# Kernel tuning notes

Hardware: AMD Instinct MI355X
Metric: run time of the kernel (lower is better)

## Reference

```python
import jax, jax.numpy as jnp
import numpy as np

HID = 1024
NH = 4  # heads for GAT conv1 and all attention blocks
FF = 2048
SLOPE = 0.2


def _ln(x, g, b):
    m = x.mean(-1, keepdims=True)
    v = ((x - m) ** 2).mean(-1, keepdims=True)
    return (x - m) / jnp.sqrt(v + 1e-5) * g + b


def _mha(q, k, v, in_w, in_b, out_w, out_b, nh):
    # q:[B,Lq,E], k/v:[B,Lk,E]; torch MultiheadAttention math (eval mode)
    B, Lq, E = q.shape
    hd = E // nh
    wq, wk, wv = jnp.split(in_w, 3, axis=0)
    bq, bk, bv = jnp.split(in_b, 3)
    qh = (q @ wq.T + bq).reshape(B, Lq, nh, hd)
    kh = (k @ wk.T + bk).reshape(B, -1, nh, hd)
    vh = (v @ wv.T + bv).reshape(B, -1, nh, hd)
    s = jnp.einsum('bqhd,bkhd->bhqk', qh, kh) / jnp.sqrt(jnp.asarray(hd, q.dtype))
    a = jax.nn.softmax(s, axis=-1)
    o = jnp.einsum('bhqk,bkhd->bqhd', a, vh).reshape(B, Lq, E)
    return o @ out_w.T + out_b


def _gatv2(x, edge_index, w_l, b_l, w_r, b_r, att, bias, heads, out_ch):
    # PyG GATv2Conv, flow='target_to_source': i (aggregation dst) = edge_index[0], j = edge_index[1]
    n = x.shape[0]
    dst = edge_index[0]
    src = edge_index[1]
    x_l = (x @ w_l + b_l).reshape(n, heads, out_ch)
    x_r = (x @ w_r + b_r).reshape(n, heads, out_ch)
    msg = x_l[src]                                   # [E,H,C] gathered source features
    e = jax.nn.leaky_relu(msg + x_r[dst], SLOPE)     # [E,H,C]
    alpha = (e * att).sum(-1)                        # [E,H]
    amax = jax.ops.segment_max(alpha, dst, num_segments=n)
    alpha = jnp.exp(alpha - amax[dst])
    denom = jax.ops.segment_sum(alpha, dst, num_segments=n)
    alpha = alpha / (denom[dst] + 1e-16)
    out = jax.ops.segment_sum(msg * alpha[..., None], dst, num_segments=n)
    return out.reshape(n, heads * out_ch) + bias


def setup_inputs() -> dict:
    key = jax.random.key(0)
    ks = iter(jax.random.split(key, 64))
    N, DF, B, L, E_rand = 8000, 768, 32, 14, 96000
    w = lambda *s: jax.random.normal(next(ks), s, jnp.float32) * 0.02
    z = lambda *s: jnp.zeros(s, jnp.float32)
    o = lambda *s: jnp.ones(s, jnp.float32)
    ei = jax.random.randint(next(ks), (2, E_rand), 0, N, jnp.int32)
    self_loops = jnp.tile(jnp.arange(N, dtype=jnp.int32)[None, :], (2, 1))
    inp = {
        'img_feat': jax.random.normal(next(ks), (B, HID), jnp.float32),
        'node_features': jax.random.normal(next(ks), (N, DF), jnp.float32),
        'edge_index': jnp.concatenate([ei, self_loops], axis=1),
        'target_idx': jax.random.randint(next(ks), (L,), 0, N, jnp.int32),
        # GATv2 conv1: 768 -> 4 heads x 256
        'gat1_wl': w(DF, HID), 'gat1_bl': z(HID), 'gat1_wr': w(DF, HID), 'gat1_br': z(HID),
        'gat1_att': w(NH, HID // NH), 'gat1_bias': z(HID),
        # GATv2 conv2: 1024 -> 1 head x 1024
        'gat2_wl': w(HID, HID), 'gat2_bl': z(HID), 'gat2_wr': w(HID, HID), 'gat2_br': z(HID),
        'gat2_att': w(1, HID), 'gat2_bias': z(HID),
        # cross-modal MHA + FFN layer
        'xa_in_w': w(3 * HID, HID), 'xa_in_b': z(3 * HID), 'xa_out_w': w(HID, HID), 'xa_out_b': z(HID),
        'xl_l1_w': w(FF, HID), 'xl_l1_b': z(FF), 'xl_l2_w': w(HID, FF), 'xl_l2_b': z(HID),
        'xl_n1_g': o(HID), 'xl_n1_b': z(HID), 'xl_n2_g': o(HID), 'xl_n2_b': z(HID),
        # 2-layer TransformerEncoder (stacked leading dim = layer)
        'enc_in_w': w(2, 3 * HID, HID), 'enc_in_b': z(2, 3 * HID),
        'enc_out_w': w(2, HID, HID), 'enc_out_b': z(2, HID),
        'enc_l1_w': w(2, FF, HID), 'enc_l1_b': z(2, FF),
        'enc_l2_w': w(2, HID, FF), 'enc_l2_b': z(2, HID),
        'enc_n1_g': o(2, HID), 'enc_n1_b': z(2, HID),
        'enc_n2_g': o(2, HID), 'enc_n2_b': z(2, HID),
        'cls_w': w(1, HID), 'cls_b': z(1),
    }
    return inp


def reference(img_feat, node_features, edge_index, target_idx,
              gat1_wl, gat1_bl, gat1_wr, gat1_br, gat1_att, gat1_bias,
              gat2_wl, gat2_bl, gat2_wr, gat2_br, gat2_att, gat2_bias,
              xa_in_w, xa_in_b, xa_out_w, xa_out_b,
              xl_l1_w, xl_l1_b, xl_l2_w, xl_l2_b, xl_n1_g, xl_n1_b, xl_n2_g, xl_n2_b,
              enc_in_w, enc_in_b, enc_out_w, enc_out_b, enc_l1_w, enc_l1_b, enc_l2_w, enc_l2_b,
              enc_n1_g, enc_n1_b, enc_n2_g, enc_n2_b, cls_w, cls_b):
    x = _gatv2(node_features, edge_index, gat1_wl, gat1_bl, gat1_wr, gat1_br, gat1_att, gat1_bias, NH, HID // NH)
    x = jax.nn.leaky_relu(x, SLOPE)
    x = _gatv2(x, edge_index, gat2_wl, gat2_bl, gat2_wr, gat2_br, gat2_att, gat2_bias, 1, HID)
    t = x[target_idx]                                  # [L, HID]
    B = img_feat.shape[0]
    L = t.shape[0]
    q = jnp.broadcast_to(t[None], (B, L, HID))
    kv = img_feat[:, None, :]                          # [B, 1, HID]
    attn = _mha(q, kv, kv, xa_in_w, xa_in_b, xa_out_w, xa_out_b, NH)
    src = _ln(t[None] + attn, xl_n1_g, xl_n1_b)
    ff = jax.nn.relu(src @ xl_l1_w.T + xl_l1_b) @ xl_l2_w.T + xl_l2_b
    src = _ln(src + ff, xl_n2_g, xl_n2_b)
    for i in range(2):  # TransformerEncoder, post-norm, relu, eval mode
        a = _mha(src, src, src, enc_in_w[i], enc_in_b[i], enc_out_w[i], enc_out_b[i], NH)
        src = _ln(src + a, enc_n1_g[i], enc_n1_b[i])
        f = jax.nn.relu(src @ enc_l1_w[i].T + enc_l1_b[i]) @ enc_l2_w[i].T + enc_l2_b[i]
        src = _ln(src + f, enc_n2_g[i], enc_n2_b[i])
    return (src @ cls_w.T + cls_b)[..., 0]             # [B, L]
```

## Files before the change

kernel.cpp:

```cpp
#include <hip/hip_runtime.h>
#include <hip/hip_bf16.h>

typedef __bf16 bf16;
typedef bf16 bf16x8 __attribute__((ext_vector_type(8)));
typedef bf16 bf16x4 __attribute__((ext_vector_type(4)));
typedef float f32x4 __attribute__((ext_vector_type(4)));

#define HID 1024
#define FFD 2048

typedef __attribute__((address_space(3))) void lds_void;
typedef const __attribute__((address_space(1))) void gm_void;

__device__ __forceinline__ void gload_lds16(const bf16* g, bf16* l)
{
    __builtin_amdgcn_global_load_lds((gm_void*)g, (lds_void*)l, 16, 0, 0);
}

__global__ __launch_bounds__(256) void cvt_bf16_kernel(
    const float* __restrict__ src, bf16* __restrict__ dst, long n)
{
    long i = ((long)blockIdx.x * 256 + threadIdx.x) * 4;
    if (i >= n) return;
    float4 f = *(const float4*)&src[i];
    bf16x4 v = {(bf16)f.x, (bf16)f.y, (bf16)f.z, (bf16)f.w};
    *(bf16x4*)&dst[i] = v;
}

__global__ __launch_bounds__(256) void cvt_t_bf16_kernel(
    const float* __restrict__ in, bf16* __restrict__ out, int R, int C)
{
    __shared__ bf16 tile[32][33];
    const int c0 = blockIdx.x * 32, r0 = blockIdx.y * 32;
    const int tx = threadIdx.x & 31, ty = threadIdx.x >> 5;
#pragma unroll
    for (int i = ty; i < 32; i += 8)
        tile[i][tx] = (bf16)in[(long)(r0 + i) * C + c0 + tx];
    __syncthreads();
#pragma unroll
    for (int i = ty; i < 32; i += 8)
        out[(long)(c0 + i) * R + r0 + tx] = tile[tx][i];
}

template <int ACT, int OUTBF16>
__global__ __launch_bounds__(256) void gemm_bf16_kernel(
    const bf16* __restrict__ A, const bf16* __restrict__ B,
    const float* __restrict__ bias, void* __restrict__ Cp,
    int M, int N, int K, int NB)
{
    const int total = gridDim.x;
    const int h = blockIdx.x;
    const int t = (total % 8 == 0) ? ((h & 7) * (total >> 3) + (h >> 3)) : h;
    const int bn = t % NB, bm = t / NB;

    const int tid  = threadIdx.x;
    const int lane = tid & 63, wave = tid >> 6;
    const int wr   = wave >> 1, wc = wave & 1;

    __shared__ bf16 As[128][32];
    __shared__ bf16 Bs[128][32];

    f32x4 acc[4][4] = {};

    const int srow = wave * 16 + (lane >> 2);
    const int scol = (lane & 3) << 3;
    const long ga0 = (long)min(bm * 128 + srow,      M - 1) * K + scol;
    const long ga1 = (long)min(bm * 128 + srow + 64, M - 1) * K + scol;
    const long gb0 = (long)(bn * 128 + srow)      * K + scol;
    const long gb1 = (long)(bn * 128 + srow + 64) * K + scol;
    bf16* ldsA0 = &As[0][0] + wave * 512;
    bf16* ldsA1 = &As[0][0] + 2048 + wave * 512;
    bf16* ldsB0 = &Bs[0][0] + wave * 512;
    bf16* ldsB1 = &Bs[0][0] + 2048 + wave * 512;

    const int quad = lane >> 4;
    const int mr   = lane & 15;
    const int kf   = quad * 8;

    for (int k0 = 0; k0 < K; k0 += 32) {
        gload_lds16(A + ga0 + k0, ldsA0);
        gload_lds16(A + ga1 + k0, ldsA1);
        gload_lds16(B + gb0 + k0, ldsB0);
        gload_lds16(B + gb1 + k0, ldsB1);
        __syncthreads();

        bf16x8 af[4], bfr[4];
#pragma unroll
        for (int i = 0; i < 4; ++i) af[i]  = *(const bf16x8*)&As[wr * 64 + i * 16 + mr][kf];
#pragma unroll
        for (int j = 0; j < 4; ++j) bfr[j] = *(const bf16x8*)&Bs[wc * 64 + j * 16 + mr][kf];
#pragma unroll
        for (int i = 0; i < 4; ++i)
#pragma unroll
            for (int j = 0; j < 4; ++j)
                acc[i][j] = __builtin_amdgcn_mfma_f32_16x16x32_bf16(af[i], bfr[j], acc[i][j], 0, 0, 0);
        __syncthreads();
    }

    const int crow = quad * 4;
#pragma unroll
    for (int i = 0; i < 4; ++i) {
#pragma unroll
        for (int j = 0; j < 4; ++j) {
            const int   col = bn * 128 + wc * 64 + j * 16 + mr;
            const float bv  = bias[col];
#pragma unroll
            for (int r = 0; r < 4; ++r) {
                const int row = bm * 128 + wr * 64 + i * 16 + crow + r;
                if (row < M) {
                    float v = acc[i][j][r] + bv;
                    if (ACT == 1) v = fmaxf(v, 0.f);
                    if (OUTBF16) ((bf16*)Cp)[(long)row * N + col] = (bf16)v;
                    else         ((float*)Cp)[(long)row * N + col] = v;
                }
            }
        }
    }
}

template <int KS>
__global__ __launch_bounds__(256) void gemm_sk_kernel(
    const float* __restrict__ A, const float* __restrict__ Bt,
    float* __restrict__ part, int M, int N, int K)
{
    const int tid  = threadIdx.x;
    const int bn   = blockIdx.x, bm = blockIdx.y, kz = blockIdx.z;
    const int lane = tid & 63, wave = tid >> 6;
    const int wr   = wave >> 1, wc = wave & 1;

    __shared__ bf16 As[128][40];
    __shared__ bf16 Bs[128][40];

    f32x4 acc[4][4] = {};

    const int  lr = tid >> 2;
    const int  lc = (tid & 3) << 3;
    const long a0 = (long)min(bm * 128 + lr,      M - 1) * K;
    const long a1 = (long)min(bm * 128 + lr + 64, M - 1) * K;
    const long b0 = (long)(bn * 128 + lr)      * K;
    const long b1 = (long)(bn * 128 + lr + 64) * K;

    const int quad = lane >> 4;
    const int mr   = lane & 15;
    const int kf   = quad * 8;

    const int Kc   = K / KS;
    const int kbeg = kz * Kc, kend = kbeg + Kc;

    float4 ra[4], rb[4];
    auto load_chunk = [&](int k0) {
        ra[0] = *(const float4*)&A[a0 + k0 + lc];
        ra[1] = *(const float4*)&A[a0 + k0 + lc + 4];
        ra[2] = *(const float4*)&A[a1 + k0 + lc];
        ra[3] = *(const float4*)&A[a1 + k0 + lc + 4];
        rb[0] = *(const float4*)&Bt[b0 + k0 + lc];
        rb[1] = *(const float4*)&Bt[b0 + k0 + lc + 4];
        rb[2] = *(const float4*)&Bt[b1 + k0 + lc];
        rb[3] = *(const float4*)&Bt[b1 + k0 + lc + 4];
    };

    load_chunk(kbeg);
    for (int k0 = kbeg; k0 < kend; k0 += 32) {
        {
            bf16x8 v0 = {(bf16)ra[0].x,(bf16)ra[0].y,(bf16)ra[0].z,(bf16)ra[0].w,
                         (bf16)ra[1].x,(bf16)ra[1].y,(bf16)ra[1].z,(bf16)ra[1].w};
            *(bf16x8*)&As[lr][lc] = v0;
            bf16x8 v1 = {(bf16)ra[2].x,(bf16)ra[2].y,(bf16)ra[2].z,(bf16)ra[2].w,
                         (bf16)ra[3].x,(bf16)ra[3].y,(bf16)ra[3].z,(bf16)ra[3].w};
            *(bf16x8*)&As[lr + 64][lc] = v1;
            bf16x8 v2 = {(bf16)rb[0].x,(bf16)rb[0].y,(bf16)rb[0].z,(bf16)rb[0].w,
                         (bf16)rb[1].x,(bf16)rb[1].y,(bf16)rb[1].z,(bf16)rb[1].w};
            *(bf16x8*)&Bs[lr][lc] = v2;
            bf16x8 v3 = {(bf16)rb[2].x,(bf16)rb[2].y,(bf16)rb[2].z,(bf16)rb[2].w,
                         (bf16)rb[3].x,(bf16)rb[3].y,(bf16)rb[3].z,(bf16)rb[3].w};
            *(bf16x8*)&Bs[lr + 64][lc] = v3;
        }
        __syncthreads();
        if (k0 + 32 < kend) load_chunk(k0 + 32);

        bf16x8 af[4], bfr[4];
#pragma unroll
        for (int i = 0; i < 4; ++i) af[i]  = *(const bf16x8*)&As[wr * 64 + i * 16 + mr][kf];
#pragma unroll
        for (int j = 0; j < 4; ++j) bfr[j] = *(const bf16x8*)&Bs[wc * 64 + j * 16 + mr][kf];
#pragma unroll
        for (int i = 0; i < 4; ++i)
#pragma unroll
            for (int j = 0; j < 4; ++j)
                acc[i][j] = __builtin_amdgcn_mfma_f32_16x16x32_bf16(af[i], bfr[j], acc[i][j], 0, 0, 0);
        __syncthreads();
    }

    const int crow = quad * 4;
    float* dst = part + (size_t)kz * M * N;
#pragma unroll
    for (int i = 0; i < 4; ++i) {
#pragma unroll
        for (int j = 0; j < 4; ++j) {
            const int col = bn * 128 + wc * 64 + j * 16 + mr;
#pragma unroll
            for (int r = 0; r < 4; ++r) {
                const int row = bm * 128 + wr * 64 + i * 16 + crow + r;
                if (row < M) dst[(long)row * N + col] = acc[i][j][r];
            }
        }
    }
}

template <int ACT, int KS>
__global__ __launch_bounds__(256) void sk_reduce_kernel(
    const float* __restrict__ part, const float* __restrict__ bias,
    float* __restrict__ C, long MN, int N)
{
    long i = ((long)blockIdx.x * 256 + threadIdx.x) * 4;
    if (i >= MN) return;
    float4 s = *(const float4*)&part[i];
#pragma unroll
    for (int k = 1; k < KS; ++k) {
        float4 p = *(const float4*)&part[(size_t)k * MN + i];
        s.x += p.x; s.y += p.y; s.z += p.z; s.w += p.w;
    }
    const int col = (int)(i % N);
    float4 bv = *(const float4*)&bias[col];
    s.x += bv.x; s.y += bv.y; s.z += bv.z; s.w += bv.w;
    if (ACT) {
        s.x = fmaxf(s.x, 0.f); s.y = fmaxf(s.y, 0.f);
        s.z = fmaxf(s.z, 0.f); s.w = fmaxf(s.w, 0.f);
    }
    *(float4*)&C[i] = s;
}

__device__ __forceinline__ void ln_finish(float v[4], int c0, const float* g,
                                          const float* beta, float* outrow)
{
    float s1 = v[0] + v[1] + v[2] + v[3];
    float s2 = v[0] * v[0] + v[1] * v[1] + v[2] * v[2] + v[3] * v[3];
    __shared__ float red[8];
    for (int o = 32; o; o >>= 1) { s1 += __shfl_down(s1, o); s2 += __shfl_down(s2, o); }
    const int wave = threadIdx.x >> 6, lane = threadIdx.x & 63;
    if (lane == 0) { red[wave] = s1; red[4 + wave] = s2; }
    __syncthreads();
    if (threadIdx.x == 0) {
        red[0] += red[1] + red[2] + red[3];
        red[4] += red[5] + red[6] + red[7];
    }
    __syncthreads();
    const float mean = red[0] * (1.f / HID);
    const float var  = fmaxf(red[4] * (1.f / HID) - mean * mean, 0.f);
    const float rstd = rsqrtf(var + 1e-5f);
#pragma unroll
    for (int k = 0; k < 4; ++k) {
        int c = c0 + k;
        outrow[c] = (v[k] - mean) * rstd * g[c] + beta[c];
    }
}

template <int KS>
__global__ __launch_bounds__(256) void sk_reduce_ln_kernel(
    const float* __restrict__ part, const float* __restrict__ bias,
    float* __restrict__ srcio, const float* __restrict__ g,
    const float* __restrict__ beta, long MN)
{
    const long row = blockIdx.x;
    const int c0 = threadIdx.x * 4;
    const long base = row * HID + c0;
    float4 s = *(const float4*)&part[base];
#pragma unroll
    for (int k = 1; k < KS; ++k) {
        float4 p = *(const float4*)&part[(size_t)k * MN + base];
        s.x += p.x; s.y += p.y; s.z += p.z; s.w += p.w;
    }
    float4 bv = *(const float4*)&bias[c0];
    float4 rv = *(const float4*)&srcio[base];
    float v[4] = {s.x + bv.x + rv.x, s.y + bv.y + rv.y,
                  s.z + bv.z + rv.z, s.w + bv.w + rv.w};
    ln_finish(v, c0, g, beta, srcio + row * HID);
}

__global__ void zero_i32_kernel(int* __restrict__ p, int n)
{
    int i = blockIdx.x * 256 + threadIdx.x;
    if (i < n) p[i] = 0;
}

__global__ void hist_kernel(const int* __restrict__ ei, int E, int* __restrict__ deg)
{
    int e = blockIdx.x * 256 + threadIdx.x;
    if (e < E) atomicAdd(&deg[ei[e]], 1);
}

__global__ void scan_kernel(const int* __restrict__ deg, int* __restrict__ rowstart,
                            int* __restrict__ cursor, int n)
{
    __shared__ int sm[1024];
    __shared__ int carry;
    if (threadIdx.x == 0) carry = 0;
    __syncthreads();
    for (int base = 0; base < n; base += 1024) {
        int i = base + threadIdx.x;
        int v = (i < n) ? deg[i] : 0;
        sm[threadIdx.x] = v;
        __syncthreads();
        for (int off = 1; off < 1024; off <<= 1) {
            int t = (threadIdx.x >= off) ? sm[threadIdx.x - off] : 0;
            __syncthreads();
            sm[threadIdx.x] += t;
            __syncthreads();
        }
        if (i < n) { int ex = carry + sm[threadIdx.x] - v; rowstart[i] = ex; cursor[i] = ex; }
        __syncthreads();
        if (threadIdx.x == 0) carry += sm[1023];
        __syncthreads();
    }
    if (threadIdx.x == 0) rowstart[n] = carry;
}

__global__ void scatter_kernel(const int* __restrict__ ei, int E,
                               int* __restrict__ cursor, int* __restrict__ eidx)
{
    int e = blockIdx.x * 256 + threadIdx.x;
    if (e < E) { int p = atomicAdd(&cursor[ei[e]], 1); eidx[p] = e; }
}

template <int NH, int LRELU, int OUTBF16>
__global__ __launch_bounds__(256) void gat_wave_kernel(
    const bf16* __restrict__ xl, const bf16* __restrict__ xr,
    const float* __restrict__ att,
    const int* __restrict__ ei, const int* __restrict__ rowstart,
    const int* __restrict__ eidx, const float* __restrict__ bias,
    void* __restrict__ outp, int E, int Nn)
{
    const int wave = threadIdx.x >> 6, lane = threadIdx.x & 63;
    const int n = blockIdx.x * 4 + wave;
    if (n >= Nn) return;

    const int rs = rowstart[n];
    int deg = rowstart[n + 1] - rs;
    if (deg > 128) deg = 128;

    int my_src = ei[E + eidx[min(rs + lane, E - 1)]];
    int my_src2 = 0;
    if (deg > 64) my_src2 = ei[E + eidx[min(rs + 64 + lane, E - 1)]];

    const int c0 = lane * 16;
    float xrf[16], av[16];
    {
        bf16x8 r0 = *(const bf16x8*)&xr[(long)n * HID + c0];
        bf16x8 r1 = *(const bf16x8*)&xr[(long)n * HID + c0 + 8];
#pragma unroll
        for (int t = 0; t < 8; ++t) { xrf[t] = (float)r0[t]; xrf[8 + t] = (float)r1[t]; }
        float4 t0 = *(const float4*)&att[c0],     t1 = *(const float4*)&att[c0 + 4];
        float4 t2 = *(const float4*)&att[c0 + 8], t3 = *(const float4*)&att[c0 + 12];
        av[0]=t0.x; av[1]=t0.y; av[2]=t0.z;  av[3]=t0.w;
        av[4]=t1.x; av[5]=t1.y; av[6]=t1.z;  av[7]=t1.w;
        av[8]=t2.x; av[9]=t2.y; av[10]=t2.z; av[11]=t2.w;
        av[12]=t3.x; av[13]=t3.y; av[14]=t3.z; av[15]=t3.w;
    }

    float m = -1e30f, s = 0.f;
    float acc[16];
#pragma unroll
    for (int t = 0; t < 16; ++t) acc[t] = 0.f;

    int sj = __shfl(my_src, 0);
    bf16x8 na0 = *(const bf16x8*)&xl[(long)sj * HID + c0];
    bf16x8 na1 = *(const bf16x8*)&xl[(long)sj * HID + c0 + 8];

    for (int j = 0; j < deg; ++j) {
        bf16x8 x0 = na0, x1 = na1;
        if (j + 1 < deg) {
            int msrc = (j + 1 < 64) ? my_src : my_src2;
            int sn = __shfl(msrc, (j + 1) & 63);
            na0 = *(const bf16x8*)&xl[(long)sn * HID + c0];
            na1 = *(const bf16x8*)&xl[(long)sn * HID + c0 + 8];
        }
        float xf[16];
#pragma unroll
        for (int t = 0; t < 8; ++t) { xf[t] = (float)x0[t]; xf[8 + t] = (float)x1[t]; }
        float partial = 0.f;
#pragma unroll
        for (int t = 0; t < 16; ++t) {
            float v = xf[t] + xrf[t];
            v = v > 0.f ? v : 0.2f * v;
            partial += v * av[t];
        }
        const int RW = (NH == 4) ? 16 : 64;
#pragma unroll
        for (int o = 1; o < RW; o <<= 1) partial += __shfl_xor(partial, o);
        float mn = fmaxf(m, partial);
        float f = __expf(m - mn);
        float p = __expf(partial - mn);
        s = s * f + p;
#pragma unroll
        for (int t = 0; t < 16; ++t) acc[t] = acc[t] * f + p * xf[t];
        m = mn;
    }

    const float dinv = 1.f / (s + 1e-16f);
    float bv[16];
    {
        float4 t0 = *(const float4*)&bias[c0],     t1 = *(const float4*)&bias[c0 + 4];
        float4 t2 = *(const float4*)&bias[c0 + 8], t3 = *(const float4*)&bias[c0 + 12];
        bv[0]=t0.x; bv[1]=t0.y; bv[2]=t0.z;  bv[3]=t0.w;
        bv[4]=t1.x; bv[5]=t1.y; bv[6]=t1.z;  bv[7]=t1.w;
        bv[8]=t2.x; bv[9]=t2.y; bv[10]=t2.z; bv[11]=t2.w;
        bv[12]=t3.x; bv[13]=t3.y; bv[14]=t3.z; bv[15]=t3.w;
    }
    float ov[16];
#pragma unroll
    for (int t = 0; t < 16; ++t) {
        float v = acc[t] * dinv + bv[t];
        if (LRELU) v = v > 0.f ? v : 0.2f * v;
        ov[t] = v;
    }
    if (OUTBF16) {
        bf16x8 w0, w1;
#pragma unroll
        for (int t = 0; t < 8; ++t) { w0[t] = (bf16)ov[t]; w1[t] = (bf16)ov[8 + t]; }
        *(bf16x8*)&((bf16*)outp)[(long)n * HID + c0] = w0;
        *(bf16x8*)&((bf16*)outp)[(long)n * HID + c0 + 8] = w1;
    } else {
        float* op = (float*)outp + (long)n * HID + c0;
#pragma unroll
        for (int t = 0; t < 4; ++t) {
            float4 w = {ov[t * 4], ov[t * 4 + 1], ov[t * 4 + 2], ov[t * 4 + 3]};
            *(float4*)&op[t * 4] = w;
        }
    }
}

__global__ __launch_bounds__(256) void ln_cross_kernel(
    const float* __restrict__ x2, const int* __restrict__ tidx,
    const float* __restrict__ attnb, const float* __restrict__ g,
    const float* __restrict__ beta, float* __restrict__ out, int L)
{
    const int row = blockIdx.x;
    const int b = row / L, l = row - b * L;
    const long tr = (long)tidx[l] * HID, ar = (long)b * HID;
    const int c0 = threadIdx.x * 4;
    float v[4];
#pragma unroll
    for (int k = 0; k < 4; ++k)
        v[k] = x2[tr + c0 + k] + attnb[ar + c0 + k];
    ln_finish(v, c0, g, beta, out + (long)row * HID);
}

__global__ __launch_bounds__(256) void self_attn_kernel(
    const float* __restrict__ qkv, float* __restrict__ out, int L)
{
    const int b = blockIdx.x >> 2, h = blockIdx.x & 3;
    const int tid = threadIdx.x;
    __shared__ float q[16][256], kk[16][256], vv[16][256];
    __shared__ float sc[16][16];
    for (int i = tid; i < L * 256; i += 256) {
        const int l = i >> 8, d = i & 255;
        const long rb = (long)(b * L + l) * 3072 + h * 256 + d;
        q[l][d]  = qkv[rb];
        kk[l][d] = qkv[rb + 1024];
        vv[l][d] = qkv[rb + 2048];
    }
    __syncthreads();
    if (tid < L * L) {
        const int l1 = tid / L, l2 = tid - l1 * L;
        float s = 0.f;
        for (int d = 0; d < 256; ++d) s += q[l1][d] * kk[l2][d];
        sc[l1][l2] = s * 0.0625f;
    }
    __syncthreads();
    if (tid < L) {
        float mx = -1e30f;
        for (int j = 0; j < L; ++j) mx = fmaxf(mx, sc[tid][j]);
        float ssum = 0.f;
        for (int j = 0; j < L; ++j) { float e = expf(sc[tid][j] - mx); sc[tid][j] = e; ssum += e; }
        const float inv = 1.f / ssum;
        for (int j = 0; j < L; ++j) sc[tid][j] *= inv;
    }
    __syncthreads();
    for (int l1 = 0; l1 < L; ++l1) {
        float a = 0.f;
        for (int l2 = 0; l2 < L; ++l2) a += sc[l1][l2] * vv[l2][tid];
        out[(long)(b * L + l1) * HID + h * 256 + tid] = a;
    }
}

__global__ __launch_bounds__(256) void cls_kernel(
    const float* __restrict__ src, const float* __restrict__ w,
    const float* __restrict__ b, float* __restrict__ out, int rows)
{
    const int row = blockIdx.x * 4 + (threadIdx.x >> 6);
    const int lane = threadIdx.x & 63;
    if (row >= rows) return;
    float s = 0.f;
    for (int c = lane; c < HID; c += 64) s += src[(long)row * HID + c] * w[c];
    for (int o = 32; o; o >>= 1) s += __shfl_down(s, o);
    if (lane == 0) out[row] = s + b[0];
}

extern "C" void kernel_launch(void* const* d_in, const int* in_sizes, int n_in,
                              void* d_out, int out_size, void* d_ws, size_t ws_size,
                              hipStream_t stream)
{
    const float* img_feat      = (const float*)d_in[0];
    const float* node_features = (const float*)d_in[1];
    const int*   edge_index    = (const int*)d_in[2];
    const int*   target_idx    = (const int*)d_in[3];
    const float* gat1_wl  = (const float*)d_in[4];
    const float* gat1_bl  = (const float*)d_in[5];
    const float* gat1_wr  = (const float*)d_in[6];
    const float* gat1_br  = (const float*)d_in[7];
    const float* gat1_att = (const float*)d_in[8];
    const float* gat1_bias= (const float*)d_in[9];
    const float* gat2_wl  = (const float*)d_in[10];
    const float* gat2_bl  = (const float*)d_in[11];
    const float* gat2_wr  = (const float*)d_in[12];
    const float* gat2_br  = (const float*)d_in[13];
    const float* gat2_att = (const float*)d_in[14];
    const float* gat2_bias= (const float*)d_in[15];
    const float* xa_in_w  = (const float*)d_in[16];
    const float* xa_in_b  = (const float*)d_in[17];
    const float* xa_out_w = (const float*)d_in[18];
    const float* xa_out_b = (const float*)d_in[19];
    const float* xl_l1_w  = (const float*)d_in[20];
    const float* xl_l1_b  = (const float*)d_in[21];
    const float* xl_l2_w  = (const float*)d_in[22];
    const float* xl_l2_b  = (const float*)d_in[23];
    const float* xl_n1_g  = (const float*)d_in[24];
    const float* xl_n1_b  = (const float*)d_in[25];
    const float* xl_n2_g  = (const float*)d_in[26];
    const float* xl_n2_b  = (const float*)d_in[27];
    const float* enc_in_w = (const float*)d_in[28];
    const float* enc_in_b = (const float*)d_in[29];
    const float* enc_out_w= (const float*)d_in[30];
    const float* enc_out_b= (const float*)d_in[31];
    const float* enc_l1_w = (const float*)d_in[32];
    const float* enc_l1_b = (const float*)d_in[33];
    const float* enc_l2_w = (const float*)d_in[34];
    const float* enc_l2_b = (const float*)d_in[35];
    const float* enc_n1_g = (const float*)d_in[36];
    const float* enc_n1_b = (const float*)d_in[37];
    const float* enc_n2_g = (const float*)d_in[38];
    const float* enc_n2_b = (const float*)d_in[39];
    const float* cls_w    = (const float*)d_in[40];
    const float* cls_b    = (const float*)d_in[41];

    const int DF = in_sizes[4] / HID;
    const int Nn = in_sizes[1] / DF;
    const int E  = in_sizes[2] / 2;
    const int L  = in_sizes[3];
    const int B  = in_sizes[0] / HID;
    const int R  = B * L;

    char* basep = (char*)d_ws;
    size_t off = 0;
    auto alloc = [&](size_t bytes) -> char* {
        char* r = basep + off; off += (bytes + 255) & ~(size_t)255; return r;
    };
    size_t regA_need = 0;
    {
        auto sz = [&](size_t b) { regA_need += (b + 255) & ~(size_t)255; };
        sz((size_t)Nn * DF * 2); sz((size_t)DF * HID * 2); sz((size_t)DF * HID * 2);
        sz((size_t)HID * HID * 2); sz((size_t)HID * HID * 2); sz((size_t)Nn * HID * 2);
    }
    size_t regA_bytes = regA_need > (size_t)Nn * HID * 4 ? regA_need : (size_t)Nn * HID * 4;
    char* regionA = alloc(regA_bytes);
    {
        size_t aoff = 0;
        auto allocA = [&](size_t bytes) -> char* {
            char* r = regionA + aoff; aoff += (bytes + 255) & ~(size_t)255; return r;
        };
        bf16* nfb  = (bf16*)allocA((size_t)Nn * DF * 2);
        bf16* w1lT = (bf16*)allocA((size_t)DF * HID * 2);
        bf16* w1rT = (bf16*)allocA((size_t)DF * HID * 2);
        bf16* w2lT = (bf16*)allocA((size_t)HID * HID * 2);
        bf16* w2rT = (bf16*)allocA((size_t)HID * HID * 2);
        bf16* x1   = (bf16*)allocA((size_t)Nn * HID * 2);

        float* x2  = (float*)regionA;

        bf16* xlb = (bf16*)alloc((size_t)Nn * HID * 2);
        bf16* xrb = (bf16*)alloc((size_t)Nn * HID * 2);
        int*   deg      = (int*)alloc((size_t)Nn * 4);
        int*   rowstart = (int*)alloc((size_t)(Nn + 1) * 4);
        int*   cursor   = (int*)alloc((size_t)(Nn + 1) * 4);
        int*   eidx     = (int*)alloc((size_t)E * 4);
        float* skpart   = (float*)alloc((size_t)8 * R * 3 * HID * 4);

        char* qb = (char*)xlb; size_t qoff = 0;
        auto alloc2 = [&](size_t bytes) -> char* {
            char* r = qb + qoff; qoff += (bytes + 255) & ~(size_t)255; return r;
        };
        float* vproj  = (float*)alloc2((size_t)B * HID * 4);
        float* attnb  = (float*)alloc2((size_t)B * HID * 4);
        float* srcbuf = (float*)alloc2((size_t)R * HID * 4);
        float* h1buf  = (float*)alloc2((size_t)R * FFD * 4);
        float* ffbuf  = (float*)alloc2((size_t)R * HID * 4);
        float* qkvbuf = (float*)alloc2((size_t)R * 3 * HID * 4);

        const int gE  = (E + 255) / 256;
        const int gMn = (Nn + 127) / 128;
        const long MNr = (long)R * HID;

        auto gemm_sk4 = [&](const float* A, const float* Bt, const float* bias,
                            float* C, int M, int N, int K, int act) {
            gemm_sk_kernel<4><<<dim3(N / 128, (M + 127) / 128, 4), 256, 0, stream>>>(
                A, Bt, skpart, M, N, K);
            long MN = (long)M * N;
            int g = (int)((MN / 4 + 255) / 256);
            if (act) sk_reduce_kernel<1,4><<<g, 256, 0, stream>>>(skpart, bias, C, MN, N);
            else     sk_reduce_kernel<0,4><<<g, 256, 0, stream>>>(skpart, bias, C, MN, N);
        };
        auto gemm_sk8 = [&](const float* A, const float* Bt, const float* bias,
                            float* C, int M, int N, int K, int act) {
            gemm_sk_kernel<8><<<dim3(N / 128, (M + 127) / 128, 8), 256, 0, stream>>>(
                A, Bt, skpart, M, N, K);
            long MN = (long)M * N;
            int g = (int)((MN / 4 + 255) / 256);
            if (act) sk_reduce_kernel<1,8><<<g, 256, 0, stream>>>(skpart, bias, C, MN, N);
            else     sk_reduce_kernel<0,8><<<g, 256, 0, stream>>>(skpart, bias, C, MN, N);
        };
        auto gemm_sk8_ln = [&](const float* A, const float* Bt, const float* bias,
                               float* srcio, const float* g, const float* beta, int K) {
            gemm_sk_kernel<8><<<dim3(HID / 128, (R + 127) / 128, 8), 256, 0, stream>>>(
                A, Bt, skpart, R, HID, K);
            sk_reduce_ln_kernel<8><<<R, 256, 0, stream>>>(skpart, bias, srcio, g, beta, MNr);
        };

        zero_i32_kernel<<<(Nn + 255) / 256, 256, 0, stream>>>(deg, Nn);
        hist_kernel<<<gE, 256, 0, stream>>>(edge_index, E, deg);
        scan_kernel<<<1, 1024, 0, stream>>>(deg, rowstart, cursor, Nn);
        scatter_kernel<<<gE, 256, 0, stream>>>(edge_index, E, cursor, eidx);

        cvt_bf16_kernel<<<(int)(((long)Nn * DF / 4 + 255) / 256), 256, 0, stream>>>(
            node_features, nfb, (long)Nn * DF);
        cvt_t_bf16_kernel<<<dim3(HID / 32, DF / 32), 256, 0, stream>>>(gat1_wl, w1lT, DF, HID);
        cvt_t_bf16_kernel<<<dim3(HID / 32, DF / 32), 256, 0, stream>>>(gat1_wr, w1rT, DF, HID);
        cvt_t_bf16_kernel<<<dim3(HID / 32, HID / 32), 256, 0, stream>>>(gat2_wl, w2lT, HID, HID);
        cvt_t_bf16_kernel<<<dim3(HID / 32, HID / 32), 256, 0, stream>>>(gat2_wr, w2rT, HID, HID);

        gemm_bf16_kernel<0,1><<<8 * gMn, 256, 0, stream>>>(nfb, w1lT, gat1_bl, xlb, Nn, HID, DF, 8);
        gemm_bf16_kernel<0,1><<<8 * gMn, 256, 0, stream>>>(nfb, w1rT, gat1_br, xrb, Nn, HID, DF, 8);
        gat_wave_kernel<4,1,1><<<(Nn + 3) / 4, 256, 0, stream>>>(
            xlb, xrb, gat1_att, edge_index, rowstart, eidx, gat1_bias, x1, E, Nn);

        gemm_bf16_kernel<0,1><<<8 * gMn, 256, 0, stream>>>(x1, w2lT, gat2_bl, xlb, Nn, HID, HID, 8);
        gemm_bf16_kernel<0,1><<<8 * gMn, 256, 0, stream>>>(x1, w2rT, gat2_br, xrb, Nn, HID, HID, 8);
        gat_wave_kernel<1,0,0><<<(Nn + 3) / 4, 256, 0, stream>>>(
            xlb, xrb, gat2_att, edge_index, rowstart, eidx, gat2_bias, x2, E, Nn);

        gemm_sk8(img_feat, xa_in_w + (size_t)2 * HID * HID, xa_in_b + 2 * HID, vproj, B, HID, HID, 0);
        gemm_sk8(vproj, xa_out_w, xa_out_b, attnb, B, HID, HID, 0);
        ln_cross_kernel<<<R, 256, 0, stream>>>(x2, target_idx, attnb, xl_n1_g, xl_n1_b, srcbuf, L);

        gemm_sk4(srcbuf, xl_l1_w, xl_l1_b, h1buf, R, FFD, HID, 1);
        gemm_sk8_ln(h1buf, xl_l2_w, xl_l2_b, srcbuf, xl_n2_g, xl_n2_b, FFD);

        for (int i = 0; i < 2; ++i) {
            gemm_sk4(srcbuf, enc_in_w + (size_t)i * 3 * HID * HID, enc_in_b + i * 3 * HID,
                     qkvbuf, R, 3 * HID, HID, 0);
            self_attn_kernel<<<B * 4, 256, 0, stream>>>(qkvbuf, ffbuf, L);
            gemm_sk8_ln(ffbuf, enc_out_w + (size_t)i * HID * HID, enc_out_b + i * HID,
                        srcbuf, enc_n1_g + i * HID, enc_n1_b + i * HID, HID);
            gemm_sk4(srcbuf, enc_l1_w + (size_t)i * FFD * HID, enc_l1_b + i * FFD,
                     h1buf, R, FFD, HID, 1);
            gemm_sk8_ln(h1buf, enc_l2_w + (size_t)i * HID * FFD, enc_l2_b + i * HID,
                        srcbuf, enc_n2_g + i * HID, enc_n2_b + i * HID, FFD);
        }

        cls_kernel<<<(R + 3) / 4, 256, 0, stream>>>(srcbuf, cls_w, cls_b, (float*)d_out, R);
    }
}
```

Before: 696.6 us.

## Restrict GATv2 layers to the two-hop neighborhood of target nodes

Only the target rows of the second GAT layer feed the rest of the model. The change builds one-hop and two-hop frontiers from the CSR adjacency, compacts them into index lists with maps, and gathers and converts only the node features it needs. The left and right projection GEMMs and both GAT aggregations then run on these compacted sets. GEMMs read the row count on the device and exit early for unused blocks. This removes most of the full-graph GEMM and aggregation work, at the cost of several small frontier and compaction launches and atomics that make row ordering nondeterministic.

```diff
diff --git a/kernel.cpp b/kernel.cpp
--- a/kernel.cpp
+++ b/kernel.cpp
@@ -17,16 +17,6 @@
     __builtin_amdgcn_global_load_lds((gm_void*)g, (lds_void*)l, 16, 0, 0);
 }
 
-__global__ __launch_bounds__(256) void cvt_bf16_kernel(
-    const float* __restrict__ src, bf16* __restrict__ dst, long n)
-{
-    long i = ((long)blockIdx.x * 256 + threadIdx.x) * 4;
-    if (i >= n) return;
-    float4 f = *(const float4*)&src[i];
-    bf16x4 v = {(bf16)f.x, (bf16)f.y, (bf16)f.z, (bf16)f.w};
-    *(bf16x4*)&dst[i] = v;
-}
-
 __global__ __launch_bounds__(256) void cvt_t_bf16_kernel(
     const float* __restrict__ in, bf16* __restrict__ out, int R, int C)
 {
@@ -46,13 +36,17 @@
 __global__ __launch_bounds__(256) void gemm_bf16_kernel(
     const bf16* __restrict__ A, const bf16* __restrict__ B,
     const float* __restrict__ bias, void* __restrict__ Cp,
-    int M, int N, int K, int NB)
+    int M, int N, int K, int NB, const int* __restrict__ cntp)
 {
     const int total = gridDim.x;
     const int h = blockIdx.x;
     const int t = (total % 8 == 0) ? ((h & 7) * (total >> 3) + (h >> 3)) : h;
     const int bn = t % NB, bm = t / NB;
 
+    int Meff = M;
+    if (cntp) Meff = *cntp;
+    if (bm * 128 >= Meff) return;
+
     const int tid  = threadIdx.x;
     const int lane = tid & 63, wave = tid >> 6;
     const int wr   = wave >> 1, wc = wave & 1;
@@ -64,8 +58,8 @@
 
     const int srow = wave * 16 + (lane >> 2);
     const int scol = (lane & 3) << 3;
-    const long ga0 = (long)min(bm * 128 + srow,      M - 1) * K + scol;
-    const long ga1 = (long)min(bm * 128 + srow + 64, M - 1) * K + scol;
+    const long ga0 = (long)min(bm * 128 + srow,      Meff - 1) * K + scol;
+    const long ga1 = (long)min(bm * 128 + srow + 64, Meff - 1) * K + scol;
     const long gb0 = (long)(bn * 128 + srow)      * K + scol;
     const long gb1 = (long)(bn * 128 + srow + 64) * K + scol;
     bf16* ldsA0 = &As[0][0] + wave * 512;
@@ -107,7 +101,7 @@
 #pragma unroll
             for (int r = 0; r < 4; ++r) {
                 const int row = bm * 128 + wr * 64 + i * 16 + crow + r;
-                if (row < M) {
+                if (row < Meff) {
                     float v = acc[i][j][r] + bv;
                     if (ACT == 1) v = fmaxf(v, 0.f);
                     if (OUTBF16) ((bf16*)Cp)[(long)row * N + col] = (bf16)v;
@@ -322,31 +316,96 @@
     if (e < E) { int p = atomicAdd(&cursor[ei[e]], 1); eidx[p] = e; }
 }
 
-template <int NH, int LRELU, int OUTBF16>
-__global__ __launch_bounds__(256) void gat_wave_kernel(
+__global__ __launch_bounds__(256) void frontier0_kernel(
+    const int* __restrict__ target_idx, int L, const int* __restrict__ rowstart,
+    const int* __restrict__ eidx, const int* __restrict__ ei, int E,
+    int* __restrict__ f1)
+{
+    const int wave = threadIdx.x >> 6, lane = threadIdx.x & 63;
+    const int w = blockIdx.x * 4 + wave;
+    if (w >= L) return;
+    const int n = target_idx[w];
+    if (lane == 0) f1[n] = 1;
+    const int rs = rowstart[n];
+    int deg = rowstart[n + 1] - rs;
+    if (deg > 128) deg = 128;
+    for (int j = lane; j < deg; j += 64)
+        f1[ei[E + eidx[rs + j]]] = 1;
+}
+
+__global__ __launch_bounds__(256) void frontier1_kernel(
+    const int* __restrict__ list1, const int* __restrict__ cnt1p,
+    const int* __restrict__ rowstart, const int* __restrict__ eidx,
+    const int* __restrict__ ei, int E, int* __restrict__ f2)
+{
+    const int wave = threadIdx.x >> 6, lane = threadIdx.x & 63;
+    const int w = blockIdx.x * 4 + wave;
+    if (w >= *cnt1p) return;
+    const int n = list1[w];
+    if (lane == 0) f2[n] = 1;
+    const int rs = rowstart[n];
+    int deg = rowstart[n + 1] - rs;
+    if (deg > 128) deg = 128;
+    for (int j = lane; j < deg; j += 64)
+        f2[ei[E + eidx[rs + j]]] = 1;
+}
+
+__global__ __launch_bounds__(256) void compact_kernel(
+    const int* __restrict__ flags, int* __restrict__ map, int* __restrict__ list,
+    int* __restrict__ cnt, int n)
+{
+    int i = blockIdx.x * 256 + threadIdx.x;
+    if (i < n && flags[i]) {
+        int p = atomicAdd(cnt, 1);
+        list[p] = i;
+        map[i] = p;
+    }
+}
+
+__global__ __launch_bounds__(256) void gather_cvt_kernel(
+    const float* __restrict__ src, bf16* __restrict__ dst,
+    const int* __restrict__ list, const int* __restrict__ cntp, int C)
+{
+    const int r = blockIdx.x;
+    if (r >= *cntp) return;
+    const long i = (long)list[r] * C;
+    const long o = (long)r * C;
+    for (int c = threadIdx.x * 4; c < C; c += 1024) {
+        float4 f = *(const float4*)&src[i + c];
+        bf16x4 v = {(bf16)f.x, (bf16)f.y, (bf16)f.z, (bf16)f.w};
+        *(bf16x4*)&dst[o + c] = v;
+    }
+}
+
+template <int NH, int LRELU, int OUTBF16, int XRMAP>
+__global__ __launch_bounds__(256) void gat_wave_idx_kernel(
     const bf16* __restrict__ xl, const bf16* __restrict__ xr,
     const float* __restrict__ att,
     const int* __restrict__ ei, const int* __restrict__ rowstart,
-    const int* __restrict__ eidx, const float* __restrict__ bias,
-    void* __restrict__ outp, int E, int Nn)
+    const int* __restrict__ eidx, const int* __restrict__ srcmap,
+    const int* __restrict__ nodelist, const int* __restrict__ cntp, int Nhost,
+    const float* __restrict__ bias, void* __restrict__ outp, int E)
 {
     const int wave = threadIdx.x >> 6, lane = threadIdx.x & 63;
-    const int n = blockIdx.x * 4 + wave;
-    if (n >= Nn) return;
+    const int w = blockIdx.x * 4 + wave;
+    const int cnt = cntp ? *cntp : Nhost;
+    if (w >= cnt) return;
+    const int n = nodelist[w];
 
     const int rs = rowstart[n];
     int deg = rowstart[n + 1] - rs;
     if (deg > 128) deg = 128;
 
-    int my_src = ei[E + eidx[min(rs + lane, E - 1)]];
+    int my_src = srcmap[ei[E + eidx[min(rs + lane, E - 1)]]];
     int my_src2 = 0;
-    if (deg > 64) my_src2 = ei[E + eidx[min(rs + 64 + lane, E - 1)]];
-
+    if (deg > 64) my_src2 = srcmap[ei[E + eidx[min(rs + 64 + lane, E - 1)]]];
+
+    const int xrrow = XRMAP ? srcmap[n] : w;
     const int c0 = lane * 16;
     float xrf[16], av[16];
     {
-        bf16x8 r0 = *(const bf16x8*)&xr[(long)n * HID + c0];
-        bf16x8 r1 = *(const bf16x8*)&xr[(long)n * HID + c0 + 8];
+        bf16x8 r0 = *(const bf16x8*)&xr[(long)xrrow * HID + c0];
+        bf16x8 r1 = *(const bf16x8*)&xr[(long)xrrow * HID + c0 + 8];
 #pragma unroll
         for (int t = 0; t < 8; ++t) { xrf[t] = (float)r0[t]; xrf[8 + t] = (float)r1[t]; }
         float4 t0 = *(const float4*)&att[c0],     t1 = *(const float4*)&att[c0 + 4];
@@ -417,31 +476,31 @@
         bf16x8 w0, w1;
 #pragma unroll
         for (int t = 0; t < 8; ++t) { w0[t] = (bf16)ov[t]; w1[t] = (bf16)ov[8 + t]; }
-        *(bf16x8*)&((bf16*)outp)[(long)n * HID + c0] = w0;
-        *(bf16x8*)&((bf16*)outp)[(long)n * HID + c0 + 8] = w1;
+        *(bf16x8*)&((bf16*)outp)[(long)w * HID + c0] = w0;
+        *(bf16x8*)&((bf16*)outp)[(long)w * HID + c0 + 8] = w1;
     } else {
-        float* op = (float*)outp + (long)n * HID + c0;
+        float* op = (float*)outp + (long)w * HID + c0;
 #pragma unroll
         for (int t = 0; t < 4; ++t) {
-            float4 w = {ov[t * 4], ov[t * 4 + 1], ov[t * 4 + 2], ov[t * 4 + 3]};
-            *(float4*)&op[t * 4] = w;
+            float4 wv = {ov[t * 4], ov[t * 4 + 1], ov[t * 4 + 2], ov[t * 4 + 3]};
+            *(float4*)&op[t * 4] = wv;
         }
     }
 }
 
 __global__ __launch_bounds__(256) void ln_cross_kernel(
-    const float* __restrict__ x2, const int* __restrict__ tidx,
-    const float* __restrict__ attnb, const float* __restrict__ g,
-    const float* __restrict__ beta, float* __restrict__ out, int L)
+    const float* __restrict__ x2c, const float* __restrict__ attnb,
+    const float* __restrict__ g, const float* __restrict__ beta,
+    float* __restrict__ out, int L)
 {
     const int row = blockIdx.x;
     const int b = row / L, l = row - b * L;
-    const long tr = (long)tidx[l] * HID, ar = (long)b * HID;
+    const long tr = (long)l * HID, ar = (long)b * HID;
     const int c0 = threadIdx.x * 4;
     float v[4];
 #pragma unroll
     for (int k = 0; k < 4; ++k)
-        v[k] = x2[tr + c0 + k] + attnb[ar + c0 + k];
+        v[k] = x2c[tr + c0 + k] + attnb[ar + c0 + k];
     ln_finish(v, c0, g, beta, out + (long)row * HID);
 }
 
@@ -550,42 +609,44 @@
     const int B  = in_sizes[0] / HID;
     const int R  = B * L;
 
+    const int cap1 = ((L * 129 + 127) / 128) * 128;
+
     char* basep = (char*)d_ws;
     size_t off = 0;
     auto alloc = [&](size_t bytes) -> char* {
         char* r = basep + off; off += (bytes + 255) & ~(size_t)255; return r;
     };
-    size_t regA_need = 0;
+
+    bf16* w1lT = (bf16*)alloc((size_t)DF * HID * 2);
+    bf16* w1rT = (bf16*)alloc((size_t)DF * HID * 2);
+    bf16* w2lT = (bf16*)alloc((size_t)HID * HID * 2);
+    bf16* w2rT = (bf16*)alloc((size_t)HID * HID * 2);
+
+    int*   deg      = (int*)alloc((size_t)Nn * 4);
+    int*   rowstart = (int*)alloc((size_t)(Nn + 1) * 4);
+    int*   cursor   = (int*)alloc((size_t)(Nn + 1) * 4);
+    int*   eidx     = (int*)alloc((size_t)E * 4);
+
+    int*   fbuf = (int*)alloc((size_t)(2 * Nn + 8) * 4);
+    int*   f1 = fbuf, *f2 = fbuf + Nn;
+    int*   cnt1 = fbuf + 2 * Nn, *cnt2 = fbuf + 2 * Nn + 1;
+    int*   map1  = (int*)alloc((size_t)Nn * 4);
+    int*   map2  = (int*)alloc((size_t)Nn * 4);
+    int*   list1 = (int*)alloc((size_t)cap1 * 4);
+    int*   list2 = (int*)alloc((size_t)Nn * 4);
+
+    bf16* nf1c = (bf16*)alloc((size_t)cap1 * DF * 2);
+    bf16* nf2c = (bf16*)alloc((size_t)Nn * DF * 2);
+    bf16* xrc  = (bf16*)alloc((size_t)cap1 * HID * 2);
+    bf16* xlc  = (bf16*)alloc((size_t)Nn * HID * 2);
+    bf16* x1c  = (bf16*)alloc((size_t)cap1 * HID * 2);
+    bf16* xl2c = (bf16*)alloc((size_t)cap1 * HID * 2);
+    bf16* xr2c = (bf16*)alloc((size_t)cap1 * HID * 2);
+    float* x2c = (float*)alloc((size_t)L * HID * 4);
+    float* skpart = (float*)alloc((size_t)8 * R * 3 * HID * 4);
+
     {
-        auto sz = [&](size_t b) { regA_need += (b + 255) & ~(size_t)255; };
-        sz((size_t)Nn * DF * 2); sz((size_t)DF * HID * 2); sz((size_t)DF * HID * 2);
-        sz((size_t)HID * HID * 2); sz((size_t)HID * HID * 2); sz((size_t)Nn * HID * 2);
-    }
-    size_t regA_bytes = regA_need > (size_t)Nn * HID * 4 ? regA_need : (size_t)Nn * HID * 4;
-    char* regionA = alloc(regA_bytes);
-    {
-        size_t aoff = 0;
-        auto allocA = [&](size_t bytes) -> char* {
-            char* r = regionA + aoff; aoff += (bytes + 255) & ~(size_t)255; return r;
-        };
-        bf16* nfb  = (bf16*)allocA((size_t)Nn * DF * 2);
-        bf16* w1lT = (bf16*)allocA((size_t)DF * HID * 2);
-        bf16* w1rT = (bf16*)allocA((size_t)DF * HID * 2);
-        bf16* w2lT = (bf16*)allocA((size_t)HID * HID * 2);
-        bf16* w2rT = (bf16*)allocA((size_t)HID * HID * 2);
-        bf16* x1   = (bf16*)allocA((size_t)Nn * HID * 2);
-
-        float* x2  = (float*)regionA;
-
-        bf16* xlb = (bf16*)alloc((size_t)Nn * HID * 2);
-        bf16* xrb = (bf16*)alloc((size_t)Nn * HID * 2);
-        int*   deg      = (int*)alloc((size_t)Nn * 4);
-        int*   rowstart = (int*)alloc((size_t)(Nn + 1) * 4);
-        int*   cursor   = (int*)alloc((size_t)(Nn + 1) * 4);
-        int*   eidx     = (int*)alloc((size_t)E * 4);
-        float* skpart   = (float*)alloc((size_t)8 * R * 3 * HID * 4);
-
-        char* qb = (char*)xlb; size_t qoff = 0;
+        char* qb = (char*)xlc; size_t qoff = 0;
         auto alloc2 = [&](size_t bytes) -> char* {
             char* r = qb + qoff; qoff += (bytes + 255) & ~(size_t)255; return r;
         };
@@ -597,8 +658,9 @@
         float* qkvbuf = (float*)alloc2((size_t)R * 3 * HID * 4);
 
         const int gE  = (E + 255) / 256;
-        const int gMn = (Nn + 127) / 128;
         const long MNr = (long)R * HID;
+        const int gMn2 = (Nn + 127) / 128;
+        const int gMn1 = (cap1 + 127) / 128;
 
         auto gemm_sk4 = [&](const float* A, const float* Bt, const float* bias,
                             float* C, int M, int N, int K, int act) {
@@ -630,26 +692,41 @@
         scan_kernel<<<1, 1024, 0, stream>>>(deg, rowstart, cursor, Nn);
         scatter_kernel<<<gE, 256, 0, stream>>>(edge_index, E, cursor, eidx);
 
-        cvt_bf16_kernel<<<(int)(((long)Nn * DF / 4 + 255) / 256), 256, 0, stream>>>(
-            node_features, nfb, (long)Nn * DF);
         cvt_t_bf16_kernel<<<dim3(HID / 32, DF / 32), 256, 0, stream>>>(gat1_wl, w1lT, DF, HID);
         cvt_t_bf16_kernel<<<dim3(HID / 32, DF / 32), 256, 0, stream>>>(gat1_wr, w1rT, DF, HID);
         cvt_t_bf16_kernel<<<dim3(HID / 32, HID / 32), 256, 0, stream>>>(gat2_wl, w2lT, HID, HID);
         cvt_t_bf16_kernel<<<dim3(HID / 32, HID / 32), 256, 0, stream>>>(gat2_wr, w2rT, HID, HID);
 
-        gemm_bf16_kernel<0,1><<<8 * gMn, 256, 0, stream>>>(nfb, w1lT, gat1_bl, xlb, Nn, HID, DF, 8);
-        gemm_bf16_kernel<0,1><<<8 * gMn, 256, 0, stream>>>(nfb, w1rT, gat1_br, xrb, Nn, HID, DF, 8);
-        gat_wave_kernel<4,1,1><<<(Nn + 3) / 4, 256, 0, stream>>>(
-            xlb, xrb, gat1_att, edge_index, rowstart, eidx, gat1_bias, x1, E, Nn);
-
-        gemm_bf16_kernel<0,1><<<8 * gMn, 256, 0, stream>>>(x1, w2lT, gat2_bl, xlb, Nn, HID, HID, 8);
-        gemm_bf16_kernel<0,1><<<8 * gMn, 256, 0, stream>>>(x1, w2rT, gat2_br, xrb, Nn, HID, HID, 8);
-        gat_wave_kernel<1,0,0><<<(Nn + 3) / 4, 256, 0, stream>>>(
-            xlb, xrb, gat2_att, edge_index, rowstart, eidx, gat2_bias, x2, E, Nn);
+        zero_i32_kernel<<<(2 * Nn + 8 + 255) / 256, 256, 0, stream>>>(fbuf, 2 * Nn + 8);
+        frontier0_kernel<<<(L + 3) / 4, 256, 0, stream>>>(
+            target_idx, L, rowstart, eidx, edge_index, E, f1);
+        compact_kernel<<<(Nn + 255) / 256, 256, 0, stream>>>(f1, map1, list1, cnt1, Nn);
+        frontier1_kernel<<<cap1 / 4, 256, 0, stream>>>(
+            list1, cnt1, rowstart, eidx, edge_index, E, f2);
+        compact_kernel<<<(Nn + 255) / 256, 256, 0, stream>>>(f2, map2, list2, cnt2, Nn);
+
+        gather_cvt_kernel<<<Nn, 256, 0, stream>>>(node_features, nf2c, list2, cnt2, DF);
+        gather_cvt_kernel<<<cap1, 256, 0, stream>>>(node_features, nf1c, list1, cnt1, DF);
+
+        gemm_bf16_kernel<0,1><<<8 * gMn2, 256, 0, stream>>>(
+            nf2c, w1lT, gat1_bl, xlc, Nn, HID, DF, 8, cnt2);
+        gemm_bf16_kernel<0,1><<<8 * gMn1, 256, 0, stream>>>(
+            nf1c, w1rT, gat1_br, xrc, cap1, HID, DF, 8, cnt1);
+        gat_wave_idx_kernel<4,1,1,0><<<cap1 / 4, 256, 0, stream>>>(
+            xlc, xrc, gat1_att, edge_index, rowstart, eidx, map2, list1, cnt1, 0,
+            gat1_bias, x1c, E);
+
+        gemm_bf16_kernel<0,1><<<8 * gMn1, 256, 0, stream>>>(
+            x1c, w2lT, gat2_bl, xl2c, cap1, HID, HID, 8, cnt1);
+        gemm_bf16_kernel<0,1><<<8 * gMn1, 256, 0, stream>>>(
+            x1c, w2rT, gat2_br, xr2c, cap1, HID, HID, 8, cnt1);
+        gat_wave_idx_kernel<1,0,0,1><<<(L + 3) / 4, 256, 0, stream>>>(
+            xl2c, xr2c, gat2_att, edge_index, rowstart, eidx, map1, target_idx,
+            nullptr, L, gat2_bias, x2c, E);
 
         gemm_sk8(img_feat, xa_in_w + (size_t)2 * HID * HID, xa_in_b + 2 * HID, vproj, B, HID, HID, 0);
         gemm_sk8(vproj, xa_out_w, xa_out_b, attnb, B, HID, HID, 0);
-        ln_cross_kernel<<<R, 256, 0, stream>>>(x2, target_idx, attnb, xl_n1_g, xl_n1_b, srcbuf, L);
+        ln_cross_kernel<<<R, 256, 0, stream>>>(x2c, attnb, xl_n1_g, xl_n1_b, srcbuf, L);
 
         gemm_sk4(srcbuf, xl_l1_w, xl_l1_b, h1buf, R, FFD, HID, 1);
         gemm_sk8_ln(h1buf, xl_l2_w, xl_l2_b, srcbuf, xl_n2_g, xl_n2_b, FFD);
```

Measured after the change: 646.8 us. 7.2% less time.
